# Kernel optimization log

Hardware: AMD Instinct MI355X
Metric: run time of the kernel (lower is better)

Reference implementation:

```python
import jax, jax.numpy as jnp
import numpy as np
from jax import lax

B = 32; P = 16; W = 6; D = 768; DEPTH = 12; K = 5
DI = 1536; DCONV = 1792; NH = 8; HD = 192; DS = 128; NC = 100; NP = 301


def setup_inputs() -> dict:
    key = jax.random.key(0)
    ks = iter(jax.random.split(key, 64))
    n = lambda shape, s=1.0: jax.random.normal(next(ks), shape, dtype=jnp.float32) * s
    return {
        "x": n((B, 1, P, W)),
        "history_feature": n((B, 1, D)),
        "patch_w": n((D, P), 0.05), "patch_b": n((D,), 0.05),
        "cnn_w": n((4, D, D, K), 0.02), "cnn_b": n((4, D), 0.02),
        "bn_g": n((4, D), 0.1) + 1.0, "bn_b": n((4, D), 0.1),
        "bn_rm": n((4, D), 0.1),
        "bn_rv": jax.random.uniform(next(ks), (4, D), dtype=jnp.float32) + 0.5,
        "cnn_state": n((4, B, D, K - 1)),
        "pos_embed": n((1, NP, D), 0.02),
        "in_proj_w": n((DEPTH, 2 * DI + 2 * DS + NH, D), 0.02),
        "conv1d_w": n((DEPTH, DCONV, 4), 0.1),
        "conv1d_b": n((DEPTH, DCONV), 0.1),
        "A_log": n((DEPTH, NH), 0.5),
        "dt_bias": n((DEPTH, NH), 0.5),
        "D_param": n((DEPTH, NH), 0.5),
        "norm_w": n((DEPTH, DI), 0.1) + 1.0,
        "out_proj_w": n((DEPTH, D, DI), 0.02),
        "mamba_conv_state": n((DEPTH, B, DCONV, 4)),
        "ssm_state": n((DEPTH, B, NH, HD, DS), 0.1),
        "fcn_g": n((D,), 0.1) + 1.0, "fcn_b": n((D,), 0.1),
        "fc_w": n((NC, D), 0.05), "fc_b": n((NC,), 0.05),
        "position_index": 10,
    }


def _cbr(h, st, w, b, g, bb, rm, rv):
    # streaming causal conv step: prepend cached K-1 samples, valid conv keeps length
    h = jnp.concatenate([st, h], axis=-1)
    h = lax.conv_general_dilated(h, w, (1,), 'VALID',
                                 dimension_numbers=('NCH', 'OIH', 'NCH')) + b[None, :, None]
    h = (h - rm[None, :, None]) / jnp.sqrt(rv[None, :, None] + 1e-5) * g[None, :, None] + bb[None, :, None]
    return jax.nn.relu(h)


def _mamba_step(tok, w_in, cw, cb, a_log, dtb, dpar, nw, w_out, conv_st, ssm_st):
    # single-token Mamba2 step (mamba_ssm semantics) with cached conv/ssm state
    zxbcdt = tok @ w_in.T                                  # [B, 3336]
    z = zxbcdt[:, :DI]
    xBC = zxbcdt[:, DI:DI + DCONV]
    dt = zxbcdt[:, DI + DCONV:]
    cs = jnp.concatenate([conv_st[:, :, 1:], xBC[:, :, None]], axis=-1)  # roll conv cache
    xBC = jax.nn.silu(jnp.sum(cs * cw[None], axis=-1) + cb)
    xin = xBC[:, :DI]
    Bm = xBC[:, DI:DI + DS]
    Cm = xBC[:, DI + DS:]
    dt = jax.nn.softplus(dt + dtb)                          # [B, NH]
    dA = jnp.exp(dt * (-jnp.exp(a_log)))                    # [B, NH]
    xh = xin.reshape(-1, NH, HD)
    st = ssm_st * dA[:, :, None, None] + jnp.einsum('bh,bn,bhp->bhpn', dt, Bm, xh)
    y = jnp.einsum('bhpn,bn->bhp', st, Cm) + dpar[None, :, None] * xh
    y = y.reshape(-1, DI) * jax.nn.silu(z)                  # gated RMSNorm
    y = y * jax.lax.rsqrt(jnp.mean(y * y, axis=-1, keepdims=True) + 1e-5) * nw
    return y @ w_out.T


def _forward(x, history_feature, patch_w, patch_b, cnn_w, cnn_b, bn_g, bn_b, bn_rm, bn_rv,
             cnn_state, pos_embed, in_proj_w, conv1d_w, conv1d_b, A_log, dt_bias, D_param,
             norm_w, out_proj_w, mamba_conv_state, ssm_state, fcn_g, fcn_b, fc_w, fc_b,
             position_index):
    # patch embed: Conv2d kernel (P,1) on [B,1,P,W] -> [B,D,W]
    h = jnp.einsum('bpw,dp->bdw', x[:, 0], patch_w) + patch_b[None, :, None]
    h = _cbr(h, cnn_state[0], cnn_w[0], cnn_b[0], bn_g[0], bn_b[0], bn_rm[0], bn_rv[0])
    h = _cbr(h, cnn_state[1], cnn_w[1], cnn_b[1], bn_g[1], bn_b[1], bn_rm[1], bn_rv[1])
    b_, d_, l_ = h.shape
    h = h.reshape(b_, d_, l_ // 3, 3).max(-1)              # MaxPool1d(3)
    h = _cbr(h, cnn_state[2], cnn_w[2], cnn_b[2], bn_g[2], bn_b[2], bn_rm[2], bn_rv[2])
    h = _cbr(h, cnn_state[3], cnn_w[3], cnn_b[3], bn_g[3], bn_b[3], bn_rm[3], bn_rv[3])
    b_, d_, l_ = h.shape
    h = h.reshape(b_, d_, l_ // 2, 2).max(-1)              # MaxPool1d(2) -> length 1
    t = h.transpose(0, 2, 1)                               # [B,1,D]
    clip = min(int(position_index), 299)
    t = t + pos_embed[:, 1 + clip, :]                      # [1,D] broadcast
    tok = t[:, 0, :]
    for i in range(DEPTH):
        tok = _mamba_step(tok, in_proj_w[i], conv1d_w[i], conv1d_b[i], A_log[i], dt_bias[i],
                          D_param[i], norm_w[i], out_proj_w[i], mamba_conv_state[i],
                          ssm_state[i]) + tok
    t = tok[:, None, :]
    mu = t.mean(-1, keepdims=True)
    var = ((t - mu) ** 2).mean(-1, keepdims=True)
    t = (t - mu) / jnp.sqrt(var + 1e-5) * fcn_g + fcn_b    # fc_norm
    history = (history_feature * position_index + t) / (position_index + 1)
    logits = history @ fc_w.T + fc_b                        # [B,1,NC]
    return logits, history


def reference(x, history_feature, patch_w, patch_b, cnn_w, cnn_b, bn_g, bn_b, bn_rm, bn_rv,
              cnn_state, pos_embed, in_proj_w, conv1d_w, conv1d_b, A_log, dt_bias, D_param,
              norm_w, out_proj_w, mamba_conv_state, ssm_state, fcn_g, fcn_b, fc_w, fc_b,
              position_index):
    return _forward(x, history_feature, patch_w, patch_b, cnn_w, cnn_b, bn_g, bn_b, bn_rm,
                    bn_rv, cnn_state, pos_embed, in_proj_w, conv1d_w, conv1d_b, A_log,
                    dt_bias, D_param, norm_w, out_proj_w, mamba_conv_state, ssm_state,
                    fcn_g, fcn_b, fc_w, fc_b, position_index)
```

## Files before the change

### kernel.cpp

```cpp
#include <hip/hip_runtime.h>
#include <math.h>

#define BB     32
#define DD     768
#define DIi    1536
#define DCONVi 1792
#define NHi    8
#define HDi    192
#define DSi    128
#define NCi    100
#define RIN    3336
#define NLAYER 12

static __device__ __forceinline__ float siluf(float x) { return x / (1.0f + expf(-x)); }

__global__ __launch_bounds__(256) void k_patch(const float* __restrict__ x,
                                               const float* __restrict__ pw,
                                               const float* __restrict__ pb,
                                               const float* __restrict__ cst0,
                                               float* __restrict__ cin0) {
  int idx = blockIdx.x * 256 + threadIdx.x;
  if (idx >= BB * DD * 10) return;
  int l = idx % 10;
  int d = (idx / 10) % DD;
  int b = idx / (10 * DD);
  float v;
  if (l < 4) {
    v = cst0[(b * DD + d) * 4 + l];
  } else {
    int w = l - 4;
    float acc = pb[d];
#pragma unroll
    for (int p = 0; p < 16; p++) acc += x[b * 96 + p * 6 + w] * pw[d * 16 + p];
    v = acc;
  }
  cin0[idx] = v;
}

template <int LIN, int LOUT>
__global__ __launch_bounds__(128) void k_conv(const float* __restrict__ cin,
                                              const float* __restrict__ w,
                                              float* __restrict__ part) {
  const int NN = BB * LOUT;
  __shared__ float Wl[16][8][5];
  __shared__ float Il[8][BB][LIN];
  int tid = threadIdx.x;
  int m0 = blockIdx.x * 16;
  int di0 = blockIdx.y * 48;
  int tm = tid >> 4;
  int tb = tid & 15;
  float acc[2][2][LOUT] = {};

  for (int cc = 0; cc < 6; cc++) {
    int dib = di0 + cc * 8;
    {
      int m = tid >> 3, di = tid & 7;
      const float* wp = w + (size_t)(m0 + m) * (DD * 5) + (dib + di) * 5;
#pragma unroll
      for (int k = 0; k < 5; k++) Wl[m][di][k] = wp[k];
    }
#pragma unroll
    for (int j = 0; j < 2; j++) {
      int flat = tid + 128 * j;
      int di = flat >> 5, b = flat & 31;
      const float* ip = cin + (size_t)(b * DD + dib + di) * LIN;
#pragma unroll
      for (int l = 0; l < LIN; l++) Il[di][b][l] = ip[l];
    }
    __syncthreads();
#pragma unroll
    for (int di = 0; di < 8; di++) {
      float a0[LIN], a1[LIN];
#pragma unroll
      for (int l = 0; l < LIN; l++) { a0[l] = Il[di][2 * tb][l]; a1[l] = Il[di][2 * tb + 1][l]; }
      float w0[5], w1[5];
#pragma unroll
      for (int k = 0; k < 5; k++) { w0[k] = Wl[2 * tm][di][k]; w1[k] = Wl[2 * tm + 1][di][k]; }
#pragma unroll
      for (int l = 0; l < LOUT; l++)
#pragma unroll
        for (int k = 0; k < 5; k++) {
          acc[0][0][l] += w0[k] * a0[l + k];
          acc[0][1][l] += w0[k] * a1[l + k];
          acc[1][0][l] += w1[k] * a0[l + k];
          acc[1][1][l] += w1[k] * a1[l + k];
        }
    }
    __syncthreads();
  }
#pragma unroll
  for (int mm = 0; mm < 2; mm++)
#pragma unroll
    for (int bb2 = 0; bb2 < 2; bb2++)
#pragma unroll
      for (int l = 0; l < LOUT; l++) {
        int d_ = m0 + 2 * tm + mm;
        int n = (2 * tb + bb2) * LOUT + l;
        part[((size_t)blockIdx.y * DD + d_) * NN + n] = acc[mm][bb2][l];
      }
}

__global__ __launch_bounds__(256) void k_bnrelu(const float* __restrict__ part, int LOUT, int PF,
                                                const float* __restrict__ cb,
                                                const float* __restrict__ bg,
                                                const float* __restrict__ bbeta,
                                                const float* __restrict__ rm,
                                                const float* __restrict__ rv, int mode,
                                                float* __restrict__ outp, int LINn,
                                                const float* __restrict__ stn,
                                                const float* __restrict__ pos,
                                                const int* __restrict__ pidx) {
  int idx = blockIdx.x * 256 + threadIdx.x;
  if (idx >= BB * DD) return;
  int d = idx % DD, b = idx / DD;
  int NN = BB * LOUT;
  float inv = rsqrtf(rv[d] + 1e-5f);
  float v[6];
  for (int l = 0; l < LOUT; l++) {
    float s = cb[d];
    for (int ss = 0; ss < 16; ss++) s += part[((size_t)ss * DD + d) * NN + b * LOUT + l];
    s = (s - rm[d]) * inv * bg[d] + bbeta[d];
    v[l] = fmaxf(s, 0.0f);
  }
  int LP = LOUT / PF;
  float pm[6];
  for (int lp = 0; lp < LP; lp++) {
    float m = v[lp * PF];
    for (int j = 1; j < PF; j++) m = fmaxf(m, v[lp * PF + j]);
    pm[lp] = m;
  }
  if (mode == 0) {
    float* o = outp + (size_t)(b * DD + d) * LINn;
    for (int j = 0; j < 4; j++) o[j] = stn[(b * DD + d) * 4 + j];
    for (int lp = 0; lp < LP; lp++) o[4 + lp] = pm[lp];
  } else {
    int clip = min(*pidx, 299);
    outp[b * DD + d] = pm[0] + pos[(1 + clip) * DD + d];
  }
}

__global__ __launch_bounds__(128) void k_inproj(const float* __restrict__ W,
                                                const float* __restrict__ tokrd,
                                                const float* __restrict__ dp, int use_dp,
                                                float* __restrict__ tokwr,
                                                float* __restrict__ zx, float* __restrict__ sq) {
  __shared__ float Wl[64][36];
  __shared__ float Tl[64][36];
  int tid = threadIdx.x;
  int m0 = blockIdx.x * 32;
  int by = blockIdx.y;
  if (blockIdx.x == 0 && by == 0 && tid < 32) sq[tid] = 0.0f;
  int tm = tid & 15, tb = tid >> 4;
  float acc[2][4] = {};
  for (int c = 0; c < 3; c++) {
    int k0 = by * 192 + c * 64;
#pragma unroll
    for (int j = 0; j < 4; j++) {
      int flat = tid + 128 * j;
      int m = flat >> 4, kf = flat & 15;
      float4 w4 = {0.f, 0.f, 0.f, 0.f};
      if (m0 + m < RIN) w4 = *(const float4*)(W + (size_t)(m0 + m) * DD + k0 + kf * 4);
      Wl[kf * 4 + 0][m] = w4.x; Wl[kf * 4 + 1][m] = w4.y;
      Wl[kf * 4 + 2][m] = w4.z; Wl[kf * 4 + 3][m] = w4.w;
    }
#pragma unroll
    for (int j = 0; j < 4; j++) {
      int flat = tid + 128 * j;
      int b = flat >> 4, kf = flat & 15;
      int off = b * DD + k0 + kf * 4;
      float4 t4 = *(const float4*)(tokrd + off);
      if (use_dp) {
#pragma unroll
        for (int s = 0; s < 4; s++) {
          float4 d4 = *(const float4*)(dp + (size_t)s * (BB * DD) + off);
          t4.x += d4.x; t4.y += d4.y; t4.z += d4.z; t4.w += d4.w;
        }
        if ((int)blockIdx.x == by) *(float4*)(tokwr + off) = t4;
      }
      Tl[kf * 4 + 0][b] = t4.x; Tl[kf * 4 + 1][b] = t4.y;
      Tl[kf * 4 + 2][b] = t4.z; Tl[kf * 4 + 3][b] = t4.w;
    }
    __syncthreads();
#pragma unroll 4
    for (int kk = 0; kk < 64; kk++) {
      float2 wv = *(const float2*)&Wl[kk][2 * tm];
      float4 tv = *(const float4*)&Tl[kk][4 * tb];
      acc[0][0] += wv.x * tv.x; acc[0][1] += wv.x * tv.y;
      acc[0][2] += wv.x * tv.z; acc[0][3] += wv.x * tv.w;
      acc[1][0] += wv.y * tv.x; acc[1][1] += wv.y * tv.y;
      acc[1][2] += wv.y * tv.z; acc[1][3] += wv.y * tv.w;
    }
    __syncthreads();
  }
#pragma unroll
  for (int mm = 0; mm < 2; mm++)
#pragma unroll
    for (int b2 = 0; b2 < 4; b2++) {
      int r = m0 + 2 * tm + mm;
      if (r < RIN) zx[((size_t)by * BB + 4 * tb + b2) * RIN + r] = acc[mm][b2];
    }
}

__global__ __launch_bounds__(256) void k_ssm(const float* __restrict__ zx,
                                             const float* __restrict__ ssm,
                                             const float* __restrict__ cst,
                                             const float* __restrict__ cw,
                                             const float* __restrict__ cb,
                                             const float* __restrict__ alog,
                                             const float* __restrict__ dtb,
                                             const float* __restrict__ dpar,
                                             float* __restrict__ y, float* __restrict__ sq) {
  int bx = blockIdx.x;
  int b = bx / 24;
  int rem = bx % 24;
  int h = rem / 3;
  int pc = rem % 3;
  int p0 = pc * 64;
  __shared__ float Cl[DSi], Bl[DSi], pl[DSi], xhl[64], zsl[64];
  __shared__ float s_dt, s_dA, s_coef;
  __shared__ float sqw[4];
  int tid = threadIdx.x;

  auto convgate = [&](int c) -> float {
    float zr = 0.f;
#pragma unroll
    for (int s = 0; s < 4; s++) zr += zx[(size_t)s * (BB * RIN) + b * RIN + (DIi + c)];
    const float* cs = cst + (size_t)(b * DCONVi + c) * 4;
    const float* wc = cw + (size_t)c * 4;
    float v = cs[1] * wc[0] + cs[2] * wc[1] + cs[3] * wc[2] + zr * wc[3] + cb[c];
    return siluf(v);
  };

  if (tid < 128) Cl[tid] = convgate(DIi + DSi + tid);
  else Bl[tid - 128] = convgate(DIi + (tid - 128));
  __syncthreads();
  if (tid < 128) {
    pl[tid] = Bl[tid] * Cl[tid];
  } else if (tid < 192) {
    int p = tid - 128;
    xhl[p] = convgate(h * HDi + p0 + p);
  } else {
    int p = tid - 192;
    float zr = 0.f;
#pragma unroll
    for (int s = 0; s < 4; s++) zr += zx[(size_t)s * (BB * RIN) + b * RIN + (h * HDi + p0 + p)];
    zsl[p] = siluf(zr);
  }
  if (tid == 0) {
    float zr = 0.f;
#pragma unroll
    for (int s = 0; s < 4; s++) zr += zx[(size_t)s * (BB * RIN) + b * RIN + (DIi + DCONVi + h)];
    float xdt = zr + dtb[h];
    float dt = fmaxf(xdt, 0.f) + log1pf(expf(-fabsf(xdt)));
    s_dt = dt;
    s_dA = expf(-expf(alog[h]) * dt);
  }
  __syncthreads();
  if (tid < 64) {
    float v = pl[tid] + pl[tid + 64];
#pragma unroll
    for (int m = 1; m < 64; m <<= 1) v += __shfl_xor(v, m, 64);
    if (tid == 0) s_coef = s_dt * v + dpar[h];
  }
  __syncthreads();

  float dA = s_dA, coef = s_coef;
  int wv = tid >> 6, lane = tid & 63;
  float c0 = Cl[2 * lane], c1 = Cl[2 * lane + 1];
  float gsq = 0.f;
  const float* sb = ssm + (size_t)((b * NHi + h) * HDi) * DSi;
  for (int i = 0; i < 16; i++) {
    int p = p0 + wv * 16 + i;
    float2 v = *(const float2*)(sb + (size_t)p * DSi + 2 * lane);
    float s = v.x * c0 + v.y * c1;
#pragma unroll
    for (int m = 1; m < 64; m <<= 1) s += __shfl_xor(s, m, 64);
    float yv = dA * s + coef * xhl[p - p0];
    if (lane == 0) {
      y[b * DIi + h * HDi + p] = yv;
      float g = yv * zsl[p - p0];
      gsq += g * g;
    }
  }
  if (lane == 0) sqw[wv] = gsq;
  __syncthreads();
  if (tid == 0) atomicAdd(&sq[b], sqw[0] + sqw[1] + sqw[2] + sqw[3]);
}

__global__ __launch_bounds__(128) void k_outproj(const float* __restrict__ W,
                                                 const float* __restrict__ y,
                                                 const float* __restrict__ zx,
                                                 const float* __restrict__ sq,
                                                 const float* __restrict__ nw,
                                                 float* __restrict__ dp) {
  __shared__ float Wl[64][20];
  __shared__ float Gl[64][36];
  __shared__ float sl[BB];
  int tid = threadIdx.x;
  if (tid < BB) sl[tid] = rsqrtf(sq[tid] * (1.0f / (float)DIi) + 1e-5f);
  __syncthreads();
  int m0 = blockIdx.x * 16, by = blockIdx.y;
  int tm = tid & 7, tb = tid >> 3;
  float acc[2][2] = {};
  for (int c = 0; c < 6; c++) {
    int k0 = by * 384 + c * 64;
#pragma unroll
    for (int j = 0; j < 2; j++) {
      int flat = tid + 128 * j;
      int m = flat >> 4, kf = flat & 15;
      float4 w4 = *(const float4*)(W + (size_t)(m0 + m) * DIi + k0 + kf * 4);
      Wl[kf * 4 + 0][m] = w4.x; Wl[kf * 4 + 1][m] = w4.y;
      Wl[kf * 4 + 2][m] = w4.z; Wl[kf * 4 + 3][m] = w4.w;
    }
#pragma unroll
    for (int j = 0; j < 4; j++) {
      int flat = tid + 128 * j;
      int b = flat >> 4, kf = flat & 15;
      int k = k0 + kf * 4;
      float4 y4 = *(const float4*)(y + b * DIi + k);
      float4 z4 = {0.f, 0.f, 0.f, 0.f};
#pragma unroll
      for (int s = 0; s < 4; s++) {
        float4 t = *(const float4*)(zx + (size_t)s * (BB * RIN) + b * RIN + k);
        z4.x += t.x; z4.y += t.y; z4.z += t.z; z4.w += t.w;
      }
      float4 n4 = *(const float4*)(nw + k);
      float sc = sl[b];
      Gl[kf * 4 + 0][b] = y4.x * siluf(z4.x) * sc * n4.x;
      Gl[kf * 4 + 1][b] = y4.y * siluf(z4.y) * sc * n4.y;
      Gl[kf * 4 + 2][b] = y4.z * siluf(z4.z) * sc * n4.z;
      Gl[kf * 4 + 3][b] = y4.w * siluf(z4.w) * sc * n4.w;
    }
    __syncthreads();
#pragma unroll 4
    for (int kk = 0; kk < 64; kk++) {
      float2 w2 = *(const float2*)&Wl[kk][2 * tm];
      float2 g2 = *(const float2*)&Gl[kk][2 * tb];
      acc[0][0] += w2.x * g2.x; acc[0][1] += w2.x * g2.y;
      acc[1][0] += w2.y * g2.x; acc[1][1] += w2.y * g2.y;
    }
    __syncthreads();
  }
#pragma unroll
  for (int mm = 0; mm < 2; mm++)
#pragma unroll
    for (int b2 = 0; b2 < 2; b2++)
      dp[((size_t)by * BB + 2 * tb + b2) * DD + m0 + 2 * tm + mm] = acc[mm][b2];
}

__global__ __launch_bounds__(256) void k_final(const float* __restrict__ tok,
                                               const float* __restrict__ dp,
                                               const float* __restrict__ hf,
                                               const float* __restrict__ fg,
                                               const float* __restrict__ fb,
                                               const float* __restrict__ fcw,
                                               const float* __restrict__ fcb,
                                               const int* __restrict__ pidx,
                                               float* __restrict__ out) {
  __shared__ float tl[DD], hl[DD], red1[4], red2[4];
  int b = blockIdx.x, tid = threadIdx.x;
  int wv = tid >> 6, lane = tid & 63;
  float psum = 0.f;
  for (int d = tid; d < DD; d += 256) {
    float v = tok[b * DD + d];
#pragma unroll
    for (int s = 0; s < 4; s++) v += dp[(size_t)s * (BB * DD) + b * DD + d];
    tl[d] = v;
    psum += v;
  }
#pragma unroll
  for (int m = 1; m < 64; m <<= 1) psum += __shfl_xor(psum, m, 64);
  if (lane == 0) red1[wv] = psum;
  __syncthreads();
  float mu = (red1[0] + red1[1] + red1[2] + red1[3]) * (1.0f / (float)DD);
  float vsum = 0.f;
  for (int d = tid; d < DD; d += 256) {
    float dd = tl[d] - mu;
    vsum += dd * dd;
  }
#pragma unroll
  for (int m = 1; m < 64; m <<= 1) vsum += __shfl_xor(vsum, m, 64);
  if (lane == 0) red2[wv] = vsum;
  __syncthreads();
  float var = (red2[0] + red2[1] + red2[2] + red2[3]) * (1.0f / (float)DD);
  float inv = rsqrtf(var + 1e-5f);
  float pi = (float)(*pidx);
  for (int d = tid; d < DD; d += 256) {
    float tn = (tl[d] - mu) * inv * fg[d] + fb[d];
    float hv = (hf[b * DD + d] * pi + tn) / (pi + 1.0f);
    hl[d] = hv;
    out[BB * NCi + b * DD + d] = hv;
  }
  __syncthreads();
  for (int n = wv; n < NCi; n += 4) {
    float s = 0.f;
    for (int d = lane; d < DD; d += 64) s += hl[d] * fcw[(size_t)n * DD + d];
#pragma unroll
    for (int m = 1; m < 64; m <<= 1) s += __shfl_xor(s, m, 64);
    if (lane == 0) out[b * NCi + n] = s + fcb[n];
  }
}

extern "C" void kernel_launch(void* const* d_in, const int* in_sizes, int n_in,
                              void* d_out, int out_size, void* d_ws, size_t ws_size,
                              hipStream_t stream) {
  const float* x       = (const float*)d_in[0];
  const float* hf      = (const float*)d_in[1];
  const float* patch_w = (const float*)d_in[2];
  const float* patch_b = (const float*)d_in[3];
  const float* cnn_w   = (const float*)d_in[4];
  const float* cnn_b   = (const float*)d_in[5];
  const float* bn_g    = (const float*)d_in[6];
  const float* bn_b    = (const float*)d_in[7];
  const float* bn_rm   = (const float*)d_in[8];
  const float* bn_rv   = (const float*)d_in[9];
  const float* cnn_st  = (const float*)d_in[10];
  const float* pos     = (const float*)d_in[11];
  const float* ipw     = (const float*)d_in[12];
  const float* cw      = (const float*)d_in[13];
  const float* cb1     = (const float*)d_in[14];
  const float* alog    = (const float*)d_in[15];
  const float* dtb     = (const float*)d_in[16];
  const float* dpar    = (const float*)d_in[17];
  const float* nw      = (const float*)d_in[18];
  const float* opw     = (const float*)d_in[19];
  const float* mcs     = (const float*)d_in[20];
  const float* ssm     = (const float*)d_in[21];
  const float* fcn_g   = (const float*)d_in[22];
  const float* fcn_b   = (const float*)d_in[23];
  const float* fc_w    = (const float*)d_in[24];
  const float* fc_b    = (const float*)d_in[25];
  const int*   pidx    = (const int*)d_in[26];
  float* out = (float*)d_out;

  float* ws = (float*)d_ws;
  float* cin0 = ws;
  float* cin1 = cin0 + 245760;
  float* cin2 = cin1 + 245760;
  float* cin3 = cin2 + 147456;
  float* part = cin3 + 147456;
  float* t0   = part + 2359296;
  float* t1   = t0 + 24576;
  float* zx   = t1 + 24576;
  float* yb   = zx + 427008;
  float* sq   = yb + 49152;
  float* dp   = sq + 32;

  k_patch<<<960, 256, 0, stream>>>(x, patch_w, patch_b, cnn_st + 0, cin0);

  k_conv<10, 6><<<dim3(48, 16), 128, 0, stream>>>(cin0, cnn_w + (size_t)0 * DD * DD * 5, part);
  k_bnrelu<<<96, 256, 0, stream>>>(part, 6, 1, cnn_b + 0 * DD, bn_g + 0 * DD, bn_b + 0 * DD,
                                   bn_rm + 0 * DD, bn_rv + 0 * DD, 0, cin1, 10,
                                   cnn_st + (size_t)1 * BB * DD * 4, pos, pidx);
  k_conv<10, 6><<<dim3(48, 16), 128, 0, stream>>>(cin1, cnn_w + (size_t)1 * DD * DD * 5, part);
  k_bnrelu<<<96, 256, 0, stream>>>(part, 6, 3, cnn_b + 1 * DD, bn_g + 1 * DD, bn_b + 1 * DD,
                                   bn_rm + 1 * DD, bn_rv + 1 * DD, 0, cin2, 6,
                                   cnn_st + (size_t)2 * BB * DD * 4, pos, pidx);
  k_conv<6, 2><<<dim3(48, 16), 128, 0, stream>>>(cin2, cnn_w + (size_t)2 * DD * DD * 5, part);
  k_bnrelu<<<96, 256, 0, stream>>>(part, 2, 1, cnn_b + 2 * DD, bn_g + 2 * DD, bn_b + 2 * DD,
                                   bn_rm + 2 * DD, bn_rv + 2 * DD, 0, cin3, 6,
                                   cnn_st + (size_t)3 * BB * DD * 4, pos, pidx);
  k_conv<6, 2><<<dim3(48, 16), 128, 0, stream>>>(cin3, cnn_w + (size_t)3 * DD * DD * 5, part);
  k_bnrelu<<<96, 256, 0, stream>>>(part, 2, 2, cnn_b + 3 * DD, bn_g + 3 * DD, bn_b + 3 * DD,
                                   bn_rm + 3 * DD, bn_rv + 3 * DD, 1, t0, 0, nullptr, pos, pidx);

  float* bufs[2] = {t0, t1};
  for (int L = 0; L < NLAYER; L++) {
    float* rd = (L == 0) ? t0 : bufs[(L + 1) & 1];
    float* wr = (L == 0) ? t1 : bufs[L & 1];
    k_inproj<<<dim3(105, 4), 128, 0, stream>>>(ipw + (size_t)L * RIN * DD, rd, dp, (L > 0) ? 1 : 0,
                                               wr, zx, sq);
    k_ssm<<<768, 256, 0, stream>>>(zx, ssm + (size_t)L * BB * NHi * HDi * DSi,
                                   mcs + (size_t)L * BB * DCONVi * 4, cw + (size_t)L * DCONVi * 4,
                                   cb1 + (size_t)L * DCONVi, alog + L * NHi, dtb + L * NHi,
                                   dpar + L * NHi, yb, sq);
    k_outproj<<<dim3(48, 4), 128, 0, stream>>>(opw + (size_t)L * DD * DIi, yb, zx, sq,
                                               nw + (size_t)L * DIi, dp);
  }

  k_final<<<32, 256, 0, stream>>>(bufs[(NLAYER - 1) & 1], dp, hf, fcn_g, fcn_b, fc_w, fc_b, pidx,
                                  out);
}
```

Baseline: 1.537 ms.

## Fuse all stages into one persistent kernel with atomic grid barriers

Replaces roughly 45 separate kernel launches with a single persistent kernel of 256 blocks. Each former kernel becomes a device phase, and phases are separated by software grid barriers built on atomic counters. Intermediate buffers change to an l-major layout, and conv, inproj and outproj tiles are re-sized for 256 threads. The aim is to remove launch overhead and inter-kernel gaps. In exchange it relies on all 256 blocks being co-resident, and the spin barriers plus a single occupancy level may limit per-phase throughput.

```diff
diff --git a/kernel.cpp b/kernel.cpp
--- a/kernel.cpp
+++ b/kernel.cpp
@@ -11,295 +11,304 @@
 #define NCi    100
 #define RIN    3336
 #define NLAYER 12
+#define NBLK   256
+#define NTHR   256
 
 static __device__ __forceinline__ float siluf(float x) { return x / (1.0f + expf(-x)); }
 
-__global__ __launch_bounds__(256) void k_patch(const float* __restrict__ x,
-                                               const float* __restrict__ pw,
-                                               const float* __restrict__ pb,
-                                               const float* __restrict__ cst0,
-                                               float* __restrict__ cin0) {
-  int idx = blockIdx.x * 256 + threadIdx.x;
-  if (idx >= BB * DD * 10) return;
-  int l = idx % 10;
-  int d = (idx / 10) % DD;
-  int b = idx / (10 * DD);
-  float v;
-  if (l < 4) {
-    v = cst0[(b * DD + d) * 4 + l];
-  } else {
-    int w = l - 4;
-    float acc = pb[d];
-#pragma unroll
-    for (int p = 0; p < 16; p++) acc += x[b * 96 + p * 6 + w] * pw[d * 16 + p];
-    v = acc;
-  }
-  cin0[idx] = v;
+static __device__ __forceinline__ void gbar(unsigned* bar, int i) {
+  __syncthreads();
+  if (threadIdx.x == 0) {
+    __hip_atomic_fetch_add(bar + i, 1u, __ATOMIC_ACQ_REL, __HIP_MEMORY_SCOPE_AGENT);
+    while (__hip_atomic_load(bar + i, __ATOMIC_ACQUIRE, __HIP_MEMORY_SCOPE_AGENT) <
+           (unsigned)NBLK) {
+      __builtin_amdgcn_s_sleep(2);
+    }
+  }
+  __syncthreads();
+}
+
+struct SmConv { float Wl[16][32][5]; float Il[16][32][10]; };
+struct SmInp  { float Wl[64][64];    float Tl[64][36]; };
+struct SmSsm  { float Cl[DSi], Bl[DSi], pl[DSi], xhl[64], zsl[64];
+                float s_dt, s_dA, s_coef, sqw[4]; };
+struct SmOut  { float Wl[2][64][20]; float Gl[2][64][36]; float sl[2][32]; };
+struct SmFin  { float tl[DD], hl[DD], red1[4], red2[4]; };
+union SmAll { SmConv c; SmInp i; SmSsm s; SmOut o; SmFin f; };
+
+static __device__ void phase_patch(const float* __restrict__ x, const float* __restrict__ pw,
+                                   const float* __restrict__ pb, const float* __restrict__ cst0,
+                                   float* __restrict__ cin0) {
+  for (int idx = blockIdx.x * NTHR + threadIdx.x; idx < 10 * BB * DD; idx += NBLK * NTHR) {
+    int d = idx % DD;
+    int b = (idx / DD) % BB;
+    int l = idx / (DD * BB);
+    float v;
+    if (l < 4) {
+      v = cst0[(b * DD + d) * 4 + l];
+    } else {
+      int w = l - 4;
+      float acc = pb[d];
+#pragma unroll
+      for (int p = 0; p < 16; p++) acc += x[b * 96 + p * 6 + w] * pw[d * 16 + p];
+      v = acc;
+    }
+    cin0[idx] = v;
+  }
 }
 
 template <int LIN, int LOUT>
-__global__ __launch_bounds__(128) void k_conv(const float* __restrict__ cin,
-                                              const float* __restrict__ w,
-                                              float* __restrict__ part) {
+static __device__ void phase_conv(SmConv& s, const float* __restrict__ cin,
+                                  const float* __restrict__ w, float* __restrict__ part) {
   const int NN = BB * LOUT;
-  __shared__ float Wl[16][8][5];
-  __shared__ float Il[8][BB][LIN];
   int tid = threadIdx.x;
-  int m0 = blockIdx.x * 16;
-  int di0 = blockIdx.y * 48;
-  int tm = tid >> 4;
-  int tb = tid & 15;
-  float acc[2][2][LOUT] = {};
-
-  for (int cc = 0; cc < 6; cc++) {
-    int dib = di0 + cc * 8;
-    {
-      int m = tid >> 3, di = tid & 7;
-      const float* wp = w + (size_t)(m0 + m) * (DD * 5) + (dib + di) * 5;
-#pragma unroll
-      for (int k = 0; k < 5; k++) Wl[m][di][k] = wp[k];
-    }
-#pragma unroll
-    for (int j = 0; j < 2; j++) {
-      int flat = tid + 128 * j;
-      int di = flat >> 5, b = flat & 31;
-      const float* ip = cin + (size_t)(b * DD + dib + di) * LIN;
-#pragma unroll
-      for (int l = 0; l < LIN; l++) Il[di][b][l] = ip[l];
-    }
+  for (int v = blockIdx.x; v < 384; v += NBLK) {
+    int bx = v % 24, by = v / 24;
+    int m0 = bx * 32, di0 = by * 48;
+    int tm = tid >> 4, tb = tid & 15;
+    float acc[2][2][LOUT] = {};
+    for (int cc = 0; cc < 3; cc++) {
+      int dib = di0 + cc * 16;
+      {
+        int m = tid >> 3, di8 = tid & 7;
+#pragma unroll
+        for (int dd = 0; dd < 2; dd++) {
+          int di = di8 + 8 * dd;
+          const float* wp = w + (size_t)(m0 + m) * (DD * 5) + (dib + di) * 5;
+#pragma unroll
+          for (int k = 0; k < 5; k++) s.Wl[di][m][k] = wp[k];
+        }
+      }
+#pragma unroll
+      for (int j = 0; j < 2; j++) {
+        int flat = tid + NTHR * j;
+        int di = flat & 15, b = flat >> 4;
+#pragma unroll
+        for (int l = 0; l < LIN; l++)
+          s.Il[di][b][l] = cin[(size_t)l * (BB * DD) + b * DD + dib + di];
+      }
+      __syncthreads();
+#pragma unroll
+      for (int di = 0; di < 16; di++) {
+        float a0[LIN], a1[LIN], w0[5], w1[5];
+#pragma unroll
+        for (int l = 0; l < LIN; l++) { a0[l] = s.Il[di][2 * tb][l]; a1[l] = s.Il[di][2 * tb + 1][l]; }
+#pragma unroll
+        for (int k = 0; k < 5; k++) { w0[k] = s.Wl[di][2 * tm][k]; w1[k] = s.Wl[di][2 * tm + 1][k]; }
+#pragma unroll
+        for (int l = 0; l < LOUT; l++)
+#pragma unroll
+          for (int k = 0; k < 5; k++) {
+            acc[0][0][l] += w0[k] * a0[l + k];
+            acc[0][1][l] += w0[k] * a1[l + k];
+            acc[1][0][l] += w1[k] * a0[l + k];
+            acc[1][1][l] += w1[k] * a1[l + k];
+          }
+      }
+      __syncthreads();
+    }
+#pragma unroll
+    for (int mm = 0; mm < 2; mm++)
+#pragma unroll
+      for (int b2 = 0; b2 < 2; b2++)
+#pragma unroll
+        for (int l = 0; l < LOUT; l++)
+          part[((size_t)by * NN + (2 * tb + b2) * LOUT + l) * DD + (m0 + 2 * tm + mm)] =
+              acc[mm][b2][l];
+  }
+}
+
+static __device__ void phase_bnrelu(int LOUT, int PF, const float* __restrict__ part,
+                                    const float* __restrict__ cb, const float* __restrict__ bg,
+                                    const float* __restrict__ bbeta, const float* __restrict__ rm,
+                                    const float* __restrict__ rv, int mode,
+                                    float* __restrict__ outp, const float* __restrict__ stn,
+                                    const float* __restrict__ pos, const int* __restrict__ pidx) {
+  int NN = BB * LOUT;
+  int idx = blockIdx.x * NTHR + threadIdx.x;
+  if (idx < BB * DD) {
+    int d = idx % DD, b = idx / DD;
+    float inv = rsqrtf(rv[d] + 1e-5f);
+    float vv[6];
+    for (int l = 0; l < LOUT; l++) {
+      float sum = cb[d];
+      for (int ss = 0; ss < 16; ss++) sum += part[((size_t)ss * NN + b * LOUT + l) * DD + d];
+      sum = (sum - rm[d]) * inv * bg[d] + bbeta[d];
+      vv[l] = fmaxf(sum, 0.0f);
+    }
+    int LP = LOUT / PF;
+    float pm[6];
+    for (int lp = 0; lp < LP; lp++) {
+      float m = vv[lp * PF];
+      for (int j = 1; j < PF; j++) m = fmaxf(m, vv[lp * PF + j]);
+      pm[lp] = m;
+    }
+    if (mode == 0) {
+      for (int j = 0; j < 4; j++) outp[(size_t)j * (BB * DD) + b * DD + d] = stn[(b * DD + d) * 4 + j];
+      for (int lp = 0; lp < LP; lp++) outp[(size_t)(4 + lp) * (BB * DD) + b * DD + d] = pm[lp];
+    } else {
+      int clip = min(*pidx, 299);
+      outp[b * DD + d] = pm[0] + pos[(1 + clip) * DD + d];
+    }
+  }
+}
+
+static __device__ void phase_inproj(SmInp& s, const float* __restrict__ W,
+                                    const float* __restrict__ tokrd, const float* __restrict__ dp,
+                                    int use_dp, float* __restrict__ tokwr, float* __restrict__ zx,
+                                    float* __restrict__ sq) {
+  int tid = threadIdx.x;
+  if (blockIdx.x == 0 && tid < BB) sq[tid] = 0.0f;
+  int v = blockIdx.x;
+  if (v < 212) {
+    int bx = v % 53, by = v / 53;
+    int m0 = bx * 64;
+    int tm = tid & 31, tb = tid >> 5;
+    float acc[2][4] = {};
+    for (int c = 0; c < 3; c++) {
+      int k0 = by * 192 + c * 64;
+#pragma unroll
+      for (int j = 0; j < 4; j++) {
+        int flat = tid + NTHR * j;
+        int m = flat >> 4, kf = flat & 15;
+        float4 w4 = {0.f, 0.f, 0.f, 0.f};
+        if (m0 + m < RIN) w4 = *(const float4*)(W + (size_t)(m0 + m) * DD + k0 + kf * 4);
+        s.Wl[kf * 4 + 0][m] = w4.x; s.Wl[kf * 4 + 1][m] = w4.y;
+        s.Wl[kf * 4 + 2][m] = w4.z; s.Wl[kf * 4 + 3][m] = w4.w;
+      }
+#pragma unroll
+      for (int j = 0; j < 2; j++) {
+        int flat = tid + NTHR * j;
+        int b = flat >> 4, kf = flat & 15;
+        int off = b * DD + k0 + kf * 4;
+        float4 t4 = *(const float4*)(tokrd + off);
+        if (use_dp) {
+#pragma unroll
+          for (int ss = 0; ss < 4; ss++) {
+            float4 d4 = *(const float4*)(dp + (size_t)ss * (BB * DD) + off);
+            t4.x += d4.x; t4.y += d4.y; t4.z += d4.z; t4.w += d4.w;
+          }
+          if (bx == by) *(float4*)(tokwr + off) = t4;
+        }
+        s.Tl[kf * 4 + 0][b] = t4.x; s.Tl[kf * 4 + 1][b] = t4.y;
+        s.Tl[kf * 4 + 2][b] = t4.z; s.Tl[kf * 4 + 3][b] = t4.w;
+      }
+      __syncthreads();
+#pragma unroll 4
+      for (int kk = 0; kk < 64; kk++) {
+        float2 wv = *(const float2*)&s.Wl[kk][2 * tm];
+        float4 tv = *(const float4*)&s.Tl[kk][4 * tb];
+        acc[0][0] += wv.x * tv.x; acc[0][1] += wv.x * tv.y;
+        acc[0][2] += wv.x * tv.z; acc[0][3] += wv.x * tv.w;
+        acc[1][0] += wv.y * tv.x; acc[1][1] += wv.y * tv.y;
+        acc[1][2] += wv.y * tv.z; acc[1][3] += wv.y * tv.w;
+      }
+      __syncthreads();
+    }
+#pragma unroll
+    for (int mm = 0; mm < 2; mm++)
+#pragma unroll
+      for (int b2 = 0; b2 < 4; b2++) {
+        int r = m0 + 2 * tm + mm;
+        if (r < RIN) zx[((size_t)by * BB + 4 * tb + b2) * RIN + r] = acc[mm][b2];
+      }
+  }
+}
+
+static __device__ void phase_ssm(SmSsm& sm, const float* __restrict__ zx,
+                                 const float* __restrict__ ssm, const float* __restrict__ cst,
+                                 const float* __restrict__ cw, const float* __restrict__ cb,
+                                 const float* __restrict__ alog, const float* __restrict__ dtb,
+                                 const float* __restrict__ dpar, float* __restrict__ y,
+                                 float* __restrict__ sq) {
+  int tid = threadIdx.x;
+  for (int v = blockIdx.x; v < 768; v += NBLK) {
+    int b = v / 24;
+    int rem = v % 24;
+    int h = rem / 3;
+    int p0 = (rem % 3) * 64;
+
+    auto convgate = [&](int c) -> float {
+      float zr = 0.f;
+#pragma unroll
+      for (int s = 0; s < 4; s++) zr += zx[(size_t)s * (BB * RIN) + b * RIN + (DIi + c)];
+      const float* cs = cst + (size_t)(b * DCONVi + c) * 4;
+      const float* wc = cw + (size_t)c * 4;
+      float val = cs[1] * wc[0] + cs[2] * wc[1] + cs[3] * wc[2] + zr * wc[3] + cb[c];
+      return siluf(val);
+    };
+
+    if (tid < 128) sm.Cl[tid] = convgate(DIi + DSi + tid);
+    else sm.Bl[tid - 128] = convgate(DIi + (tid - 128));
     __syncthreads();
-#pragma unroll
-    for (int di = 0; di < 8; di++) {
-      float a0[LIN], a1[LIN];
-#pragma unroll
-      for (int l = 0; l < LIN; l++) { a0[l] = Il[di][2 * tb][l]; a1[l] = Il[di][2 * tb + 1][l]; }
-      float w0[5], w1[5];
-#pragma unroll
-      for (int k = 0; k < 5; k++) { w0[k] = Wl[2 * tm][di][k]; w1[k] = Wl[2 * tm + 1][di][k]; }
-#pragma unroll
-      for (int l = 0; l < LOUT; l++)
-#pragma unroll
-        for (int k = 0; k < 5; k++) {
-          acc[0][0][l] += w0[k] * a0[l + k];
-          acc[0][1][l] += w0[k] * a1[l + k];
-          acc[1][0][l] += w1[k] * a0[l + k];
-          acc[1][1][l] += w1[k] * a1[l + k];
-        }
+    if (tid < 128) {
+      sm.pl[tid] = sm.Bl[tid] * sm.Cl[tid];
+    } else if (tid < 192) {
+      int p = tid - 128;
+      sm.xhl[p] = convgate(h * HDi + p0 + p);
+    } else {
+      int p = tid - 192;
+      float zr = 0.f;
+#pragma unroll
+      for (int s = 0; s < 4; s++)
+        zr += zx[(size_t)s * (BB * RIN) + b * RIN + (h * HDi + p0 + p)];
+      sm.zsl[p] = siluf(zr);
+    }
+    if (tid == 0) {
+      float zr = 0.f;
+#pragma unroll
+      for (int s = 0; s < 4; s++)
+        zr += zx[(size_t)s * (BB * RIN) + b * RIN + (DIi + DCONVi + h)];
+      float xdt = zr + dtb[h];
+      float dt = fmaxf(xdt, 0.f) + log1pf(expf(-fabsf(xdt)));
+      sm.s_dt = dt;
+      sm.s_dA = expf(-expf(alog[h]) * dt);
     }
     __syncthreads();
-  }
-#pragma unroll
-  for (int mm = 0; mm < 2; mm++)
-#pragma unroll
-    for (int bb2 = 0; bb2 < 2; bb2++)
-#pragma unroll
-      for (int l = 0; l < LOUT; l++) {
-        int d_ = m0 + 2 * tm + mm;
-        int n = (2 * tb + bb2) * LOUT + l;
-        part[((size_t)blockIdx.y * DD + d_) * NN + n] = acc[mm][bb2][l];
-      }
-}
-
-__global__ __launch_bounds__(256) void k_bnrelu(const float* __restrict__ part, int LOUT, int PF,
-                                                const float* __restrict__ cb,
-                                                const float* __restrict__ bg,
-                                                const float* __restrict__ bbeta,
-                                                const float* __restrict__ rm,
-                                                const float* __restrict__ rv, int mode,
-                                                float* __restrict__ outp, int LINn,
-                                                const float* __restrict__ stn,
-                                                const float* __restrict__ pos,
-                                                const int* __restrict__ pidx) {
-  int idx = blockIdx.x * 256 + threadIdx.x;
-  if (idx >= BB * DD) return;
-  int d = idx % DD, b = idx / DD;
-  int NN = BB * LOUT;
-  float inv = rsqrtf(rv[d] + 1e-5f);
-  float v[6];
-  for (int l = 0; l < LOUT; l++) {
-    float s = cb[d];
-    for (int ss = 0; ss < 16; ss++) s += part[((size_t)ss * DD + d) * NN + b * LOUT + l];
-    s = (s - rm[d]) * inv * bg[d] + bbeta[d];
-    v[l] = fmaxf(s, 0.0f);
-  }
-  int LP = LOUT / PF;
-  float pm[6];
-  for (int lp = 0; lp < LP; lp++) {
-    float m = v[lp * PF];
-    for (int j = 1; j < PF; j++) m = fmaxf(m, v[lp * PF + j]);
-    pm[lp] = m;
-  }
-  if (mode == 0) {
-    float* o = outp + (size_t)(b * DD + d) * LINn;
-    for (int j = 0; j < 4; j++) o[j] = stn[(b * DD + d) * 4 + j];
-    for (int lp = 0; lp < LP; lp++) o[4 + lp] = pm[lp];
-  } else {
-    int clip = min(*pidx, 299);
-    outp[b * DD + d] = pm[0] + pos[(1 + clip) * DD + d];
-  }
-}
-
-__global__ __launch_bounds__(128) void k_inproj(const float* __restrict__ W,
-                                                const float* __restrict__ tokrd,
-                                                const float* __restrict__ dp, int use_dp,
-                                                float* __restrict__ tokwr,
-                                                float* __restrict__ zx, float* __restrict__ sq) {
-  __shared__ float Wl[64][36];
-  __shared__ float Tl[64][36];
-  int tid = threadIdx.x;
-  int m0 = blockIdx.x * 32;
-  int by = blockIdx.y;
-  if (blockIdx.x == 0 && by == 0 && tid < 32) sq[tid] = 0.0f;
-  int tm = tid & 15, tb = tid >> 4;
-  float acc[2][4] = {};
-  for (int c = 0; c < 3; c++) {
-    int k0 = by * 192 + c * 64;
-#pragma unroll
-    for (int j = 0; j < 4; j++) {
-      int flat = tid + 128 * j;
-      int m = flat >> 4, kf = flat & 15;
-      float4 w4 = {0.f, 0.f, 0.f, 0.f};
-      if (m0 + m < RIN) w4 = *(const float4*)(W + (size_t)(m0 + m) * DD + k0 + kf * 4);
-      Wl[kf * 4 + 0][m] = w4.x; Wl[kf * 4 + 1][m] = w4.y;
-      Wl[kf * 4 + 2][m] = w4.z; Wl[kf * 4 + 3][m] = w4.w;
-    }
-#pragma unroll
-    for (int j = 0; j < 4; j++) {
-      int flat = tid + 128 * j;
-      int b = flat >> 4, kf = flat & 15;
-      int off = b * DD + k0 + kf * 4;
-      float4 t4 = *(const float4*)(tokrd + off);
-      if (use_dp) {
-#pragma unroll
-        for (int s = 0; s < 4; s++) {
-          float4 d4 = *(const float4*)(dp + (size_t)s * (BB * DD) + off);
-          t4.x += d4.x; t4.y += d4.y; t4.z += d4.z; t4.w += d4.w;
-        }
-        if ((int)blockIdx.x == by) *(float4*)(tokwr + off) = t4;
-      }
-      Tl[kf * 4 + 0][b] = t4.x; Tl[kf * 4 + 1][b] = t4.y;
-      Tl[kf * 4 + 2][b] = t4.z; Tl[kf * 4 + 3][b] = t4.w;
+    if (tid < 64) {
+      float pv = sm.pl[tid] + sm.pl[tid + 64];
+#pragma unroll
+      for (int m = 1; m < 64; m <<= 1) pv += __shfl_xor(pv, m, 64);
+      if (tid == 0) sm.s_coef = sm.s_dt * pv + dpar[h];
     }
     __syncthreads();
+
+    float dA = sm.s_dA, coef = sm.s_coef;
+    int wv = tid >> 6, lane = tid & 63;
+    float c0 = sm.Cl[2 * lane], c1 = sm.Cl[2 * lane + 1];
+    float gsq = 0.f;
+    const float* sb = ssm + (size_t)((b * NHi + h) * HDi) * DSi;
 #pragma unroll 4
-    for (int kk = 0; kk < 64; kk++) {
-      float2 wv = *(const float2*)&Wl[kk][2 * tm];
-      float4 tv = *(const float4*)&Tl[kk][4 * tb];
-      acc[0][0] += wv.x * tv.x; acc[0][1] += wv.x * tv.y;
-      acc[0][2] += wv.x * tv.z; acc[0][3] += wv.x * tv.w;
-      acc[1][0] += wv.y * tv.x; acc[1][1] += wv.y * tv.y;
-      acc[1][2] += wv.y * tv.z; acc[1][3] += wv.y * tv.w;
-    }
+    for (int i = 0; i < 16; i++) {
+      int p = p0 + wv * 16 + i;
+      float2 sv = *(const float2*)(sb + (size_t)p * DSi + 2 * lane);
+      float ssum = sv.x * c0 + sv.y * c1;
+#pragma unroll
+      for (int m = 1; m < 64; m <<= 1) ssum += __shfl_xor(ssum, m, 64);
+      float yv = dA * ssum + coef * sm.xhl[p - p0];
+      if (lane == 0) {
+        y[b * DIi + h * HDi + p] = yv;
+        float g = yv * sm.zsl[p - p0];
+        gsq += g * g;
+      }
+    }
+    if (lane == 0) sm.sqw[wv] = gsq;
     __syncthreads();
-  }
-#pragma unroll
-  for (int mm = 0; mm < 2; mm++)
-#pragma unroll
-    for (int b2 = 0; b2 < 4; b2++) {
-      int r = m0 + 2 * tm + mm;
-      if (r < RIN) zx[((size_t)by * BB + 4 * tb + b2) * RIN + r] = acc[mm][b2];
-    }
-}
-
-__global__ __launch_bounds__(256) void k_ssm(const float* __restrict__ zx,
-                                             const float* __restrict__ ssm,
-                                             const float* __restrict__ cst,
-                                             const float* __restrict__ cw,
-                                             const float* __restrict__ cb,
-                                             const float* __restrict__ alog,
-                                             const float* __restrict__ dtb,
-                                             const float* __restrict__ dpar,
-                                             float* __restrict__ y, float* __restrict__ sq) {
-  int bx = blockIdx.x;
-  int b = bx / 24;
-  int rem = bx % 24;
-  int h = rem / 3;
-  int pc = rem % 3;
-  int p0 = pc * 64;
-  __shared__ float Cl[DSi], Bl[DSi], pl[DSi], xhl[64], zsl[64];
-  __shared__ float s_dt, s_dA, s_coef;
-  __shared__ float sqw[4];
-  int tid = threadIdx.x;
-
-  auto convgate = [&](int c) -> float {
-    float zr = 0.f;
-#pragma unroll
-    for (int s = 0; s < 4; s++) zr += zx[(size_t)s * (BB * RIN) + b * RIN + (DIi + c)];
-    const float* cs = cst + (size_t)(b * DCONVi + c) * 4;
-    const float* wc = cw + (size_t)c * 4;
-    float v = cs[1] * wc[0] + cs[2] * wc[1] + cs[3] * wc[2] + zr * wc[3] + cb[c];
-    return siluf(v);
-  };
-
-  if (tid < 128) Cl[tid] = convgate(DIi + DSi + tid);
-  else Bl[tid - 128] = convgate(DIi + (tid - 128));
+    if (tid == 0) atomicAdd(&sq[b], sm.sqw[0] + sm.sqw[1] + sm.sqw[2] + sm.sqw[3]);
+  }
+}
+
+static __device__ void phase_outproj(SmOut& s, const float* __restrict__ W,
+                                     const float* __restrict__ y, const float* __restrict__ zx,
+                                     const float* __restrict__ sq, const float* __restrict__ nw,
+                                     float* __restrict__ dp) {
+  if (blockIdx.x >= 96) return;
+  int sub = threadIdx.x >> 7, tid = threadIdx.x & 127;
+  int vb = blockIdx.x * 2 + sub;
+  int bx = vb % 48, by = vb / 48;
+  if (tid < BB) s.sl[sub][tid] = rsqrtf(sq[tid] * (1.0f / (float)DIi) + 1e-5f);
   __syncthreads();
-  if (tid < 128) {
-    pl[tid] = Bl[tid] * Cl[tid];
-  } else if (tid < 192) {
-    int p = tid - 128;
-    xhl[p] = convgate(h * HDi + p0 + p);
-  } else {
-    int p = tid - 192;
-    float zr = 0.f;
-#pragma unroll
-    for (int s = 0; s < 4; s++) zr += zx[(size_t)s * (BB * RIN) + b * RIN + (h * HDi + p0 + p)];
-    zsl[p] = siluf(zr);
-  }
-  if (tid == 0) {
-    float zr = 0.f;
-#pragma unroll
-    for (int s = 0; s < 4; s++) zr += zx[(size_t)s * (BB * RIN) + b * RIN + (DIi + DCONVi + h)];
-    float xdt = zr + dtb[h];
-    float dt = fmaxf(xdt, 0.f) + log1pf(expf(-fabsf(xdt)));
-    s_dt = dt;
-    s_dA = expf(-expf(alog[h]) * dt);
-  }
-  __syncthreads();
-  if (tid < 64) {
-    float v = pl[tid] + pl[tid + 64];
-#pragma unroll
-    for (int m = 1; m < 64; m <<= 1) v += __shfl_xor(v, m, 64);
-    if (tid == 0) s_coef = s_dt * v + dpar[h];
-  }
-  __syncthreads();
-
-  float dA = s_dA, coef = s_coef;
-  int wv = tid >> 6, lane = tid & 63;
-  float c0 = Cl[2 * lane], c1 = Cl[2 * lane + 1];
-  float gsq = 0.f;
-  const float* sb = ssm + (size_t)((b * NHi + h) * HDi) * DSi;
-  for (int i = 0; i < 16; i++) {
-    int p = p0 + wv * 16 + i;
-    float2 v = *(const float2*)(sb + (size_t)p * DSi + 2 * lane);
-    float s = v.x * c0 + v.y * c1;
-#pragma unroll
-    for (int m = 1; m < 64; m <<= 1) s += __shfl_xor(s, m, 64);
-    float yv = dA * s + coef * xhl[p - p0];
-    if (lane == 0) {
-      y[b * DIi + h * HDi + p] = yv;
-      float g = yv * zsl[p - p0];
-      gsq += g * g;
-    }
-  }
-  if (lane == 0) sqw[wv] = gsq;
-  __syncthreads();
-  if (tid == 0) atomicAdd(&sq[b], sqw[0] + sqw[1] + sqw[2] + sqw[3]);
-}
-
-__global__ __launch_bounds__(128) void k_outproj(const float* __restrict__ W,
-                                                 const float* __restrict__ y,
-                                                 const float* __restrict__ zx,
-                                                 const float* __restrict__ sq,
-                                                 const float* __restrict__ nw,
-                                                 float* __restrict__ dp) {
-  __shared__ float Wl[64][20];
-  __shared__ float Gl[64][36];
-  __shared__ float sl[BB];
-  int tid = threadIdx.x;
-  if (tid < BB) sl[tid] = rsqrtf(sq[tid] * (1.0f / (float)DIi) + 1e-5f);
-  __syncthreads();
-  int m0 = blockIdx.x * 16, by = blockIdx.y;
+  int m0 = bx * 16;
   int tm = tid & 7, tb = tid >> 3;
   float acc[2][2] = {};
   for (int c = 0; c < 6; c++) {
@@ -309,8 +318,8 @@
       int flat = tid + 128 * j;
       int m = flat >> 4, kf = flat & 15;
       float4 w4 = *(const float4*)(W + (size_t)(m0 + m) * DIi + k0 + kf * 4);
-      Wl[kf * 4 + 0][m] = w4.x; Wl[kf * 4 + 1][m] = w4.y;
-      Wl[kf * 4 + 2][m] = w4.z; Wl[kf * 4 + 3][m] = w4.w;
+      s.Wl[sub][kf * 4 + 0][m] = w4.x; s.Wl[sub][kf * 4 + 1][m] = w4.y;
+      s.Wl[sub][kf * 4 + 2][m] = w4.z; s.Wl[sub][kf * 4 + 3][m] = w4.w;
     }
 #pragma unroll
     for (int j = 0; j < 4; j++) {
@@ -320,22 +329,22 @@
       float4 y4 = *(const float4*)(y + b * DIi + k);
       float4 z4 = {0.f, 0.f, 0.f, 0.f};
 #pragma unroll
-      for (int s = 0; s < 4; s++) {
-        float4 t = *(const float4*)(zx + (size_t)s * (BB * RIN) + b * RIN + k);
+      for (int ss = 0; ss < 4; ss++) {
+        float4 t = *(const float4*)(zx + (size_t)ss * (BB * RIN) + b * RIN + k);
         z4.x += t.x; z4.y += t.y; z4.z += t.z; z4.w += t.w;
       }
       float4 n4 = *(const float4*)(nw + k);
-      float sc = sl[b];
-      Gl[kf * 4 + 0][b] = y4.x * siluf(z4.x) * sc * n4.x;
-      Gl[kf * 4 + 1][b] = y4.y * siluf(z4.y) * sc * n4.y;
-      Gl[kf * 4 + 2][b] = y4.z * siluf(z4.z) * sc * n4.z;
-      Gl[kf * 4 + 3][b] = y4.w * siluf(z4.w) * sc * n4.w;
+      float sc = s.sl[sub][b];
+      s.Gl[sub][kf * 4 + 0][b] = y4.x * siluf(z4.x) * sc * n4.x;
+      s.Gl[sub][kf * 4 + 1][b] = y4.y * siluf(z4.y) * sc * n4.y;
+      s.Gl[sub][kf * 4 + 2][b] = y4.z * siluf(z4.z) * sc * n4.z;
+      s.Gl[sub][kf * 4 + 3][b] = y4.w * siluf(z4.w) * sc * n4.w;
     }
     __syncthreads();
 #pragma unroll 4
     for (int kk = 0; kk < 64; kk++) {
-      float2 w2 = *(const float2*)&Wl[kk][2 * tm];
-      float2 g2 = *(const float2*)&Gl[kk][2 * tb];
+      float2 w2 = *(const float2*)&s.Wl[sub][kk][2 * tm];
+      float2 g2 = *(const float2*)&s.Gl[sub][kk][2 * tb];
       acc[0][0] += w2.x * g2.x; acc[0][1] += w2.x * g2.y;
       acc[1][0] += w2.y * g2.x; acc[1][1] += w2.y * g2.y;
     }
@@ -348,57 +357,108 @@
       dp[((size_t)by * BB + 2 * tb + b2) * DD + m0 + 2 * tm + mm] = acc[mm][b2];
 }
 
-__global__ __launch_bounds__(256) void k_final(const float* __restrict__ tok,
-                                               const float* __restrict__ dp,
-                                               const float* __restrict__ hf,
-                                               const float* __restrict__ fg,
-                                               const float* __restrict__ fb,
-                                               const float* __restrict__ fcw,
-                                               const float* __restrict__ fcb,
-                                               const int* __restrict__ pidx,
-                                               float* __restrict__ out) {
-  __shared__ float tl[DD], hl[DD], red1[4], red2[4];
+static __device__ void phase_final(SmFin& s, const float* __restrict__ tok,
+                                   const float* __restrict__ dp, const float* __restrict__ hf,
+                                   const float* __restrict__ fg, const float* __restrict__ fb,
+                                   const float* __restrict__ fcw, const float* __restrict__ fcb,
+                                   const int* __restrict__ pidx, float* __restrict__ out) {
+  if (blockIdx.x >= BB) return;
   int b = blockIdx.x, tid = threadIdx.x;
   int wv = tid >> 6, lane = tid & 63;
   float psum = 0.f;
-  for (int d = tid; d < DD; d += 256) {
+  for (int d = tid; d < DD; d += NTHR) {
     float v = tok[b * DD + d];
 #pragma unroll
-    for (int s = 0; s < 4; s++) v += dp[(size_t)s * (BB * DD) + b * DD + d];
-    tl[d] = v;
+    for (int ss = 0; ss < 4; ss++) v += dp[(size_t)ss * (BB * DD) + b * DD + d];
+    s.tl[d] = v;
     psum += v;
   }
 #pragma unroll
   for (int m = 1; m < 64; m <<= 1) psum += __shfl_xor(psum, m, 64);
-  if (lane == 0) red1[wv] = psum;
+  if (lane == 0) s.red1[wv] = psum;
   __syncthreads();
-  float mu = (red1[0] + red1[1] + red1[2] + red1[3]) * (1.0f / (float)DD);
+  float mu = (s.red1[0] + s.red1[1] + s.red1[2] + s.red1[3]) * (1.0f / (float)DD);
   float vsum = 0.f;
-  for (int d = tid; d < DD; d += 256) {
-    float dd = tl[d] - mu;
+  for (int d = tid; d < DD; d += NTHR) {
+    float dd = s.tl[d] - mu;
     vsum += dd * dd;
   }
 #pragma unroll
   for (int m = 1; m < 64; m <<= 1) vsum += __shfl_xor(vsum, m, 64);
-  if (lane == 0) red2[wv] = vsum;
+  if (lane == 0) s.red2[wv] = vsum;
   __syncthreads();
-  float var = (red2[0] + red2[1] + red2[2] + red2[3]) * (1.0f / (float)DD);
+  float var = (s.red2[0] + s.red2[1] + s.red2[2] + s.red2[3]) * (1.0f / (float)DD);
   float inv = rsqrtf(var + 1e-5f);
   float pi = (float)(*pidx);
-  for (int d = tid; d < DD; d += 256) {
-    float tn = (tl[d] - mu) * inv * fg[d] + fb[d];
+  for (int d = tid; d < DD; d += NTHR) {
+    float tn = (s.tl[d] - mu) * inv * fg[d] + fb[d];
     float hv = (hf[b * DD + d] * pi + tn) / (pi + 1.0f);
-    hl[d] = hv;
+    s.hl[d] = hv;
     out[BB * NCi + b * DD + d] = hv;
   }
   __syncthreads();
   for (int n = wv; n < NCi; n += 4) {
-    float s = 0.f;
-    for (int d = lane; d < DD; d += 64) s += hl[d] * fcw[(size_t)n * DD + d];
-#pragma unroll
-    for (int m = 1; m < 64; m <<= 1) s += __shfl_xor(s, m, 64);
-    if (lane == 0) out[b * NCi + n] = s + fcb[n];
-  }
+    float sum = 0.f;
+    for (int d = lane; d < DD; d += 64) sum += s.hl[d] * fcw[(size_t)n * DD + d];
+#pragma unroll
+    for (int m = 1; m < 64; m <<= 1) sum += __shfl_xor(sum, m, 64);
+    if (lane == 0) out[b * NCi + n] = sum + fcb[n];
+  }
+}
+
+__global__ void k_zero(unsigned* bar) {
+  if (threadIdx.x < 64) bar[threadIdx.x] = 0u;
+}
+
+__global__ __launch_bounds__(NTHR, 1) void k_mega(
+    const float* x, const float* hf, const float* patch_w, const float* patch_b,
+    const float* cnn_w, const float* cnn_b, const float* bn_g, const float* bn_b,
+    const float* bn_rm, const float* bn_rv, const float* cnn_st, const float* pos,
+    const float* ipw, const float* cw, const float* cb1, const float* alog, const float* dtb,
+    const float* dpar, const float* nw, const float* opw, const float* mcs, const float* ssm,
+    const float* fcn_g, const float* fcn_b, const float* fc_w, const float* fc_b,
+    const int* pidx, float* out, float* cin0, float* cin1, float* cin2, float* cin3,
+    float* part, float* t0, float* t1, float* zx, float* yb, float* sq, float* dp,
+    unsigned* bar) {
+  __shared__ SmAll sm;
+
+  phase_patch(x, patch_w, patch_b, cnn_st, cin0);
+  gbar(bar, 0);
+  phase_conv<10, 6>(sm.c, cin0, cnn_w + (size_t)0 * DD * DD * 5, part);
+  gbar(bar, 1);
+  phase_bnrelu(6, 1, part, cnn_b, bn_g, bn_b, bn_rm, bn_rv, 0, cin1,
+               cnn_st + (size_t)1 * BB * DD * 4, pos, pidx);
+  gbar(bar, 2);
+  phase_conv<10, 6>(sm.c, cin1, cnn_w + (size_t)1 * DD * DD * 5, part);
+  gbar(bar, 3);
+  phase_bnrelu(6, 3, part, cnn_b + DD, bn_g + DD, bn_b + DD, bn_rm + DD, bn_rv + DD, 0, cin2,
+               cnn_st + (size_t)2 * BB * DD * 4, pos, pidx);
+  gbar(bar, 4);
+  phase_conv<6, 2>(sm.c, cin2, cnn_w + (size_t)2 * DD * DD * 5, part);
+  gbar(bar, 5);
+  phase_bnrelu(2, 1, part, cnn_b + 2 * DD, bn_g + 2 * DD, bn_b + 2 * DD, bn_rm + 2 * DD,
+               bn_rv + 2 * DD, 0, cin3, cnn_st + (size_t)3 * BB * DD * 4, pos, pidx);
+  gbar(bar, 6);
+  phase_conv<6, 2>(sm.c, cin3, cnn_w + (size_t)3 * DD * DD * 5, part);
+  gbar(bar, 7);
+  phase_bnrelu(2, 2, part, cnn_b + 3 * DD, bn_g + 3 * DD, bn_b + 3 * DD, bn_rm + 3 * DD,
+               bn_rv + 3 * DD, 1, t0, nullptr, pos, pidx);
+  gbar(bar, 8);
+
+  int bi = 9;
+  for (int L = 0; L < NLAYER; L++) {
+    const float* rd = (L == 0) ? t0 : ((L & 1) ? t0 : t1);
+    float* wr = (L & 1) ? t1 : ((L == 0) ? t1 : t0);
+    phase_inproj(sm.i, ipw + (size_t)L * RIN * DD, rd, dp, (L > 0) ? 1 : 0, wr, zx, sq);
+    gbar(bar, bi++);
+    phase_ssm(sm.s, zx, ssm + (size_t)L * BB * NHi * HDi * DSi, mcs + (size_t)L * BB * DCONVi * 4,
+              cw + (size_t)L * DCONVi * 4, cb1 + (size_t)L * DCONVi, alog + L * NHi,
+              dtb + L * NHi, dpar + L * NHi, yb, sq);
+    gbar(bar, bi++);
+    phase_outproj(sm.o, opw + (size_t)L * DD * DIi, yb, zx, sq, nw + (size_t)L * DIi, dp);
+    gbar(bar, bi++);
+  }
+  phase_final(sm.f, t1, dp, hf, fcn_g, fcn_b, fc_w, fc_b, pidx, out);
 }
 
 extern "C" void kernel_launch(void* const* d_in, const int* in_sizes, int n_in,
@@ -433,8 +493,9 @@
   const int*   pidx    = (const int*)d_in[26];
   float* out = (float*)d_out;
 
-  float* ws = (float*)d_ws;
-  float* cin0 = ws;
+  unsigned* bar = (unsigned*)d_ws;
+  float* fw   = (float*)d_ws + 64;
+  float* cin0 = fw;
   float* cin1 = cin0 + 245760;
   float* cin2 = cin1 + 245760;
   float* cin3 = cin2 + 147456;
@@ -446,38 +507,9 @@
   float* sq   = yb + 49152;
   float* dp   = sq + 32;
 
-  k_patch<<<960, 256, 0, stream>>>(x, patch_w, patch_b, cnn_st + 0, cin0);
-
-  k_conv<10, 6><<<dim3(48, 16), 128, 0, stream>>>(cin0, cnn_w + (size_t)0 * DD * DD * 5, part);
-  k_bnrelu<<<96, 256, 0, stream>>>(part, 6, 1, cnn_b + 0 * DD, bn_g + 0 * DD, bn_b + 0 * DD,
-                                   bn_rm + 0 * DD, bn_rv + 0 * DD, 0, cin1, 10,
-                                   cnn_st + (size_t)1 * BB * DD * 4, pos, pidx);
-  k_conv<10, 6><<<dim3(48, 16), 128, 0, stream>>>(cin1, cnn_w + (size_t)1 * DD * DD * 5, part);
-  k_bnrelu<<<96, 256, 0, stream>>>(part, 6, 3, cnn_b + 1 * DD, bn_g + 1 * DD, bn_b + 1 * DD,
-                                   bn_rm + 1 * DD, bn_rv + 1 * DD, 0, cin2, 6,
-                                   cnn_st + (size_t)2 * BB * DD * 4, pos, pidx);
-  k_conv<6, 2><<<dim3(48, 16), 128, 0, stream>>>(cin2, cnn_w + (size_t)2 * DD * DD * 5, part);
-  k_bnrelu<<<96, 256, 0, stream>>>(part, 2, 1, cnn_b + 2 * DD, bn_g + 2 * DD, bn_b + 2 * DD,
-                                   bn_rm + 2 * DD, bn_rv + 2 * DD, 0, cin3, 6,
-                                   cnn_st + (size_t)3 * BB * DD * 4, pos, pidx);
-  k_conv<6, 2><<<dim3(48, 16), 128, 0, stream>>>(cin3, cnn_w + (size_t)3 * DD * DD * 5, part);
-  k_bnrelu<<<96, 256, 0, stream>>>(part, 2, 2, cnn_b + 3 * DD, bn_g + 3 * DD, bn_b + 3 * DD,
-                                   bn_rm + 3 * DD, bn_rv + 3 * DD, 1, t0, 0, nullptr, pos, pidx);
-
-  float* bufs[2] = {t0, t1};
-  for (int L = 0; L < NLAYER; L++) {
-    float* rd = (L == 0) ? t0 : bufs[(L + 1) & 1];
-    float* wr = (L == 0) ? t1 : bufs[L & 1];
-    k_inproj<<<dim3(105, 4), 128, 0, stream>>>(ipw + (size_t)L * RIN * DD, rd, dp, (L > 0) ? 1 : 0,
-                                               wr, zx, sq);
-    k_ssm<<<768, 256, 0, stream>>>(zx, ssm + (size_t)L * BB * NHi * HDi * DSi,
-                                   mcs + (size_t)L * BB * DCONVi * 4, cw + (size_t)L * DCONVi * 4,
-                                   cb1 + (size_t)L * DCONVi, alog + L * NHi, dtb + L * NHi,
-                                   dpar + L * NHi, yb, sq);
-    k_outproj<<<dim3(48, 4), 128, 0, stream>>>(opw + (size_t)L * DD * DIi, yb, zx, sq,
-                                               nw + (size_t)L * DIi, dp);
-  }
-
-  k_final<<<32, 256, 0, stream>>>(bufs[(NLAYER - 1) & 1], dp, hf, fcn_g, fcn_b, fc_w, fc_b, pidx,
-                                  out);
-}
+  k_zero<<<1, 64, 0, stream>>>(bar);
+  k_mega<<<NBLK, NTHR, 0, stream>>>(x, hf, patch_w, patch_b, cnn_w, cnn_b, bn_g, bn_b, bn_rm,
+                                    bn_rv, cnn_st, pos, ipw, cw, cb1, alog, dtb, dpar, nw, opw,
+                                    mcs, ssm, fcn_g, fcn_b, fc_w, fc_b, pidx, out, cin0, cin1,
+                                    cin2, cin3, part, t0, t1, zx, yb, sq, dp, bar);
+}
```

Measured after the change: 3.035 ms. +97.5%, slower.
